# Kernel tuning notes

Hardware: AMD Instinct MI355X
Metric: run time of the kernel (lower is better)

## Reference

```python
import jax, jax.numpy as jnp
import numpy as np

N = 100000
E = 1600000

def _norms(src, dst):
    ones = jnp.ones(src.shape[0], dtype=jnp.float32)
    out_deg = jax.ops.segment_sum(ones, src, num_segments=N)
    in_deg = jax.ops.segment_sum(ones, dst, num_segments=N)
    # dgl clamps degree to >=1; with self-loops deg>=1 anyway
    out_norm = jax.lax.rsqrt(jnp.clip(out_deg, 1.0))
    in_norm = jax.lax.rsqrt(jnp.clip(in_deg, 1.0))
    return out_norm, in_norm

def _graph_conv(x, W, b, src, dst, out_norm, in_norm):
    h = (x * out_norm[:, None]) @ W          # [N, dout]
    msg = h[src]                              # gather  [E', dout]
    agg = jax.ops.segment_sum(msg, dst, num_segments=N)
    return agg * in_norm[:, None] + b

def setup_inputs() -> dict:
    key = jax.random.key(0)
    ks = jax.random.split(key, 8)
    feat = jax.random.normal(ks[0], (N, 128), dtype=jnp.float32)
    src = jax.random.randint(ks[1], (E,), 0, N, dtype=jnp.int32)
    dst = jax.random.randint(ks[2], (E,), 0, N, dtype=jnp.int32)
    s1 = 1.0 / np.sqrt(128.0)
    W1 = jax.random.uniform(ks[3], (128, 128), jnp.float32, -s1, s1)
    b1 = jnp.zeros((128,), jnp.float32)
    W2 = jax.random.uniform(ks[4], (128, 128), jnp.float32, -s1, s1)
    b2 = jnp.zeros((128,), jnp.float32)
    W3 = jax.random.uniform(ks[5], (128, 64), jnp.float32, -s1, s1)
    b3 = jnp.zeros((64,), jnp.float32)
    return {"feat": feat, "src": src, "dst": dst,
            "W1": W1, "b1": b1, "W2": W2, "b2": b2, "W3": W3, "b3": b3}

def reference(feat, src, dst, W1, b1, W2, b2, W3, b3):
    # dgl.add_self_loop
    loop = jnp.arange(N, dtype=src.dtype)
    s = jnp.concatenate([src, loop])
    d = jnp.concatenate([dst, loop])
    out_norm, in_norm = _norms(s, d)
    # dropout is identity in eval mode (deterministic reference)
    h = jax.nn.relu(_graph_conv(feat, W1, b1, s, d, out_norm, in_norm))
    h = jax.nn.relu(_graph_conv(h, W2, b2, s, d, out_norm, in_norm))
    h = _graph_conv(h, W3, b3, s, d, out_norm, in_norm)
    return h
```

## Files before the change

### kernel.cpp

```cpp
#include <hip/hip_runtime.h>
#include <hip/hip_fp16.h>


#define NFEAT 128
#define BBITS 8
#define BSZ 256
#define EPB 4096

union H8 { float4 f4; __half2 h2[4]; };

using half8v = __attribute__((ext_vector_type(8))) _Float16;
using f32x4  = __attribute__((ext_vector_type(4))) float;

__global__ __launch_bounds__(256) void hist_kernel(const int* __restrict__ src,
                                                   const int* __restrict__ dst,
                                                   int* __restrict__ hist2,
                                                   int NB, int nblk, int nh, int E) {
    __shared__ int hd[512], hs[512];
    const int t = threadIdx.x, b = blockIdx.x;
    for (int u = t; u < 512; u += 256) { hd[u] = 0; hs[u] = 0; }
    __syncthreads();
    const int base4 = b * (EPB / 4);
    #pragma unroll
    for (int j = 0; j < 4; ++j) {
        int i4 = base4 + j * 256 + t;
        int e0 = i4 * 4;
        if (e0 + 3 < E) {
            int4 s = ((const int4*)src)[i4];
            int4 d = ((const int4*)dst)[i4];
            atomicAdd(&hs[s.x >> BBITS], 1); atomicAdd(&hs[s.y >> BBITS], 1);
            atomicAdd(&hs[s.z >> BBITS], 1); atomicAdd(&hs[s.w >> BBITS], 1);
            atomicAdd(&hd[d.x >> BBITS], 1); atomicAdd(&hd[d.y >> BBITS], 1);
            atomicAdd(&hd[d.z >> BBITS], 1); atomicAdd(&hd[d.w >> BBITS], 1);
        } else {
            for (int e = e0; e < E && e < e0 + 4; ++e) {
                atomicAdd(&hs[src[e] >> BBITS], 1);
                atomicAdd(&hd[dst[e] >> BBITS], 1);
            }
        }
    }
    __syncthreads();
    for (int u = t; u < NB; u += 256) {
        hist2[u * nblk + b]      = hd[u];
        hist2[nh + u * nblk + b] = hs[u];
    }
}

__global__ __launch_bounds__(256) void scan1_kernel(int* __restrict__ data,
                                                    int* __restrict__ blk_sum, int n) {
    const int tid = threadIdx.x, lane = tid & 63, wid = tid >> 6;
    const int i2 = blockIdx.x * 256 + tid;
    int a = 0, b = 0;
    if (2 * i2 + 1 < n)      { int2 v = ((const int2*)data)[i2]; a = v.x; b = v.y; }
    else if (2 * i2 < n)     { a = data[2 * i2]; }
    int s = a + b;
    int incl = s;
    #pragma unroll
    for (int off = 1; off < 64; off <<= 1) {
        int t2 = __shfl_up(incl, off, 64);
        if (lane >= off) incl += t2;
    }
    __shared__ int ws[4];
    if (lane == 63) ws[wid] = incl;
    __syncthreads();
    int woff = 0;
    #pragma unroll
    for (int w = 0; w < 3; ++w) if (w < wid) woff += ws[w];
    int pref = woff + incl - s;
    if (2 * i2 < n)     data[2 * i2]     = pref;
    if (2 * i2 + 1 < n) data[2 * i2 + 1] = pref + a;
    if (tid == 0) blk_sum[blockIdx.x] = ws[0] + ws[1] + ws[2] + ws[3];
}

__global__ __launch_bounds__(1024) void scan2_kernel(int* __restrict__ blk, int nb) {
    const int tid = threadIdx.x, lane = tid & 63, wid = tid >> 6;
    int v = (tid < nb) ? blk[tid] : 0;
    int incl = v;
    #pragma unroll
    for (int off = 1; off < 64; off <<= 1) {
        int t = __shfl_up(incl, off, 64);
        if (lane >= off) incl += t;
    }
    __shared__ int ws[16];
    if (lane == 63) ws[wid] = incl;
    __syncthreads();
    int woff = 0;
    #pragma unroll
    for (int w = 0; w < 15; ++w) if (w < wid) woff += ws[w];
    if (tid < nb) blk[tid] = woff + incl - v;
}

__global__ __launch_bounds__(256) void scan3_kernel(int* __restrict__ data,
                                                    const int* __restrict__ blk, int n) {
    const int i2 = blockIdx.x * 256 + threadIdx.x;
    int add = blk[blockIdx.x];
    if (2 * i2 < n)     data[2 * i2]     += add;
    if (2 * i2 + 1 < n) data[2 * i2 + 1] += add;
}

__global__ __launch_bounds__(256) void scatter_kernel(const int* __restrict__ src,
                                                      const int* __restrict__ dst,
                                                      const int* __restrict__ hist2,
                                                      unsigned int* __restrict__ dstP,
                                                      unsigned char* __restrict__ srcB,
                                                      int NB, int nblk, int nh, int E) {
    __shared__ int hd[512], hs[512], baseD[512], baseS[512];
    const int t = threadIdx.x, b = blockIdx.x;
    for (int u = t; u < 512; u += 256) { hd[u] = 0; hs[u] = 0; }
    for (int u = t; u < NB; u += 256) {
        baseD[u] = hist2[u * nblk + b];
        baseS[u] = hist2[nh + u * nblk + b] - E;
    }
    __syncthreads();
    const int base4 = b * (EPB / 4);
    #pragma unroll
    for (int j = 0; j < 4; ++j) {
        int i4 = base4 + j * 256 + t;
        int e0 = i4 * 4;
        if (e0 + 3 < E) {
            int4 s = ((const int4*)src)[i4];
            int4 d = ((const int4*)dst)[i4];
            int se[4] = {s.x, s.y, s.z, s.w};
            int de[4] = {d.x, d.y, d.z, d.w};
            #pragma unroll
            for (int q = 0; q < 4; ++q) {
                int kd = de[q] >> BBITS;
                int pos = baseD[kd] + atomicAdd(&hd[kd], 1);
                dstP[pos] = ((unsigned int)(de[q] & (BSZ - 1)) << 24) | (unsigned int)se[q];
                int ks = se[q] >> BBITS;
                int posS = baseS[ks] + atomicAdd(&hs[ks], 1);
                srcB[posS] = (unsigned char)(se[q] & (BSZ - 1));
            }
        } else {
            for (int e = e0; e < E && e < e0 + 4; ++e) {
                int sv = src[e], dv = dst[e];
                int kd = dv >> BBITS;
                int pos = baseD[kd] + atomicAdd(&hd[kd], 1);
                dstP[pos] = ((unsigned int)(dv & (BSZ - 1)) << 24) | (unsigned int)sv;
                int ks = sv >> BBITS;
                int posS = baseS[ks] + atomicAdd(&hs[ks], 1);
                srcB[posS] = (unsigned char)(sv & (BSZ - 1));
            }
        }
    }
}

__global__ __launch_bounds__(256) void bucket_kernel(const unsigned int* __restrict__ dstP,
                                                     const unsigned char* __restrict__ srcB,
                                                     const int* __restrict__ hist2,
                                                     int* __restrict__ row_ptr,
                                                     int* __restrict__ col_idx,
                                                     float* __restrict__ in_norm,
                                                     float* __restrict__ out_norm,
                                                     int N, int NB, int nblk, int nh, int E) {
    __shared__ int cnt[BSZ], scnt[BSZ], start[BSZ], off[BSZ];
    __shared__ int ws[4];
    const int k = blockIdx.x, t = threadIdx.x;
    const int node0 = k << BBITS;
    cnt[t] = 0; scnt[t] = 0; off[t] = 0;
    __syncthreads();
    const int bB = hist2[k * nblk];
    const int bE = (k + 1 < NB) ? hist2[(k + 1) * nblk] : E;
    const int sB = hist2[nh + k * nblk] - E;
    const int sE = ((k + 1 < NB) ? hist2[nh + (k + 1) * nblk] : 2 * E) - E;
    for (int i = bB + t; i < bE; i += 256) atomicAdd(&cnt[dstP[i] >> 24], 1);
    for (int i = sB + t; i < sE; i += 256) atomicAdd(&scnt[srcB[i]], 1);
    __syncthreads();
    const int lane = t & 63, wid = t >> 6;
    int v = cnt[t];
    int incl = v;
    #pragma unroll
    for (int o = 1; o < 64; o <<= 1) {
        int x = __shfl_up(incl, o, 64);
        if (lane >= o) incl += x;
    }
    if (lane == 63) ws[wid] = incl;
    __syncthreads();
    int woff = 0;
    #pragma unroll
    for (int w = 0; w < 3; ++w) if (w < wid) woff += ws[w];
    start[t] = woff + incl - v;
    {
        int node = node0 + t;
        if (node < N) {
            row_ptr[node] = bB + start[t];
            in_norm[node]  = rsqrtf((float)(v + 1));
            out_norm[node] = rsqrtf((float)(scnt[t] + 1));
        }
    }
    if (k == 0 && t == 0) row_ptr[N] = E;
    __syncthreads();
    for (int i = bB + t; i < bE; i += 256) {
        unsigned int pv = dstP[i];
        int local = pv >> 24;
        int r = atomicAdd(&off[local], 1);
        col_idx[bB + start[local] + r] = (int)(pv & 0xFFFFFFu);
    }
}

__global__ void wt_all_kernel(const float* __restrict__ W1, const float* __restrict__ W2,
                              const float* __restrict__ W3, __half* __restrict__ Wt1,
                              __half* __restrict__ Wt2, __half* __restrict__ Wt3) {
    int b = blockIdx.x, k = threadIdx.x;
    if (b < 128)      Wt1[b * 128 + k] = __float2half(W1[k * 128 + b]);
    else if (b < 256) { int n = b - 128; Wt2[n * 128 + k] = __float2half(W2[k * 128 + n]); }
    else              { int n = b - 256; Wt3[n * 128 + k] = __float2half(W3[k * 64 + n]); }
}

template <int BN, typename XT>
__global__ __launch_bounds__(256) void mfma_gemm_kernel(const XT* __restrict__ x,
                                                        const __half* __restrict__ Wt,
                                                        const float* __restrict__ out_norm,
                                                        __half* __restrict__ h, int n_rows) {
    constexpr int BM = 64;
    constexpr int NT = BN / 16;
    __shared__ __half As[BM][136];
    __shared__ __half Bs[BN][136];
    const int tid  = threadIdx.x;
    const int row0 = blockIdx.x * BM;

    {
        int r  = tid >> 2;
        int c0 = (tid & 3) * 32;
        int grow = row0 + r;
        if (grow < n_rows) {
            float norm = out_norm[grow];
            if constexpr (sizeof(XT) == 4) {
                const float* xp = (const float*)x + (size_t)grow * NFEAT + c0;
                #pragma unroll
                for (int j = 0; j < 4; ++j) {
                    float4 p0 = *(const float4*)(xp + j * 8);
                    float4 p1 = *(const float4*)(xp + j * 8 + 4);
                    H8 u;
                    u.h2[0] = __floats2half2_rn(p0.x * norm, p0.y * norm);
                    u.h2[1] = __floats2half2_rn(p0.z * norm, p0.w * norm);
                    u.h2[2] = __floats2half2_rn(p1.x * norm, p1.y * norm);
                    u.h2[3] = __floats2half2_rn(p1.z * norm, p1.w * norm);
                    *(float4*)&As[r][c0 + j * 8] = u.f4;
                }
            } else {
                const __half* xp = (const __half*)x + (size_t)grow * NFEAT + c0;
                #pragma unroll
                for (int j = 0; j < 4; ++j) {
                    H8 u; u.f4 = *(const float4*)(xp + j * 8);
                    #pragma unroll
                    for (int q = 0; q < 4; ++q) {
                        float2 p = __half22float2(u.h2[q]);
                        u.h2[q] = __floats2half2_rn(p.x * norm, p.y * norm);
                    }
                    *(float4*)&As[r][c0 + j * 8] = u.f4;
                }
            }
        } else {
            H8 z; z.f4 = make_float4(0.f, 0.f, 0.f, 0.f);
            #pragma unroll
            for (int j = 0; j < 4; ++j) *(float4*)&As[r][c0 + j * 8] = z.f4;
        }
    }
    {
        constexpr int TPR = 256 / BN;
        constexpr int CH  = 128 / TPR;
        int wr = tid / TPR;
        int wc = (tid % TPR) * CH;
        const __half* wp = Wt + wr * 128 + wc;
        #pragma unroll
        for (int j = 0; j < CH / 8; ++j)
            *(float4*)&Bs[wr][wc + j * 8] = *(const float4*)(wp + j * 8);
    }
    __syncthreads();

    const int lane = tid & 63, wid = tid >> 6;
    const int lr = lane & 15, quad = lane >> 4;
    const int koff = quad * 8;
    f32x4 acc[NT];
    #pragma unroll
    for (int t = 0; t < NT; ++t) acc[t] = (f32x4){0.f, 0.f, 0.f, 0.f};

    #pragma unroll
    for (int ks = 0; ks < 4; ++ks) {
        half8v a = *(const half8v*)&As[wid * 16 + lr][ks * 32 + koff];
        #pragma unroll
        for (int nt = 0; nt < NT; ++nt) {
            half8v b = *(const half8v*)&Bs[nt * 16 + lr][ks * 32 + koff];
            acc[nt] = __builtin_amdgcn_mfma_f32_16x16x32_f16(a, b, acc[nt], 0, 0, 0);
        }
    }

    #pragma unroll
    for (int nt = 0; nt < NT; ++nt) {
        #pragma unroll
        for (int r = 0; r < 4; ++r) {
            int row = row0 + wid * 16 + quad * 4 + r;
            if (row < n_rows)
                h[(size_t)row * BN + nt * 16 + lr] = __float2half(acc[nt][r]);
        }
    }
}

template <int DOUT, bool RELU, typename OutT>
__global__ __launch_bounds__(256) void agg_kernel(const __half* __restrict__ h,
                                                  const int* __restrict__ row_ptr,
                                                  const int* __restrict__ col_idx,
                                                  const float* __restrict__ in_norm,
                                                  const float* __restrict__ bias,
                                                  OutT* __restrict__ out, int n) {
    constexpr int TPN = DOUT / 8;
    constexpr int NPB = 256 / TPN;
    const int tid  = threadIdx.x;
    const int sub  = tid / TPN;
    const int c    = (tid % TPN) * 8;
    const int node = blockIdx.x * NPB + sub;
    if (node >= n) return;

    float acc[8];
    {
        H8 u; u.f4 = *(const float4*)(h + (size_t)node * DOUT + c);
        #pragma unroll
        for (int q = 0; q < 4; ++q) {
            float2 p = __half22float2(u.h2[q]);
            acc[q * 2] = p.x; acc[q * 2 + 1] = p.y;
        }
    }
    int e  = row_ptr[node];
    int e1 = row_ptr[node + 1];
    for (; e + 3 < e1; e += 4) {
        int s0 = col_idx[e], s1 = col_idx[e + 1], s2 = col_idx[e + 2], s3 = col_idx[e + 3];
        H8 u0, u1, u2, u3;
        u0.f4 = *(const float4*)(h + (size_t)s0 * DOUT + c);
        u1.f4 = *(const float4*)(h + (size_t)s1 * DOUT + c);
        u2.f4 = *(const float4*)(h + (size_t)s2 * DOUT + c);
        u3.f4 = *(const float4*)(h + (size_t)s3 * DOUT + c);
        #pragma unroll
        for (int q = 0; q < 4; ++q) {
            float2 p0 = __half22float2(u0.h2[q]);
            float2 p1 = __half22float2(u1.h2[q]);
            float2 p2 = __half22float2(u2.h2[q]);
            float2 p3 = __half22float2(u3.h2[q]);
            acc[q * 2]     += (p0.x + p1.x) + (p2.x + p3.x);
            acc[q * 2 + 1] += (p0.y + p1.y) + (p2.y + p3.y);
        }
    }
    for (; e < e1; ++e) {
        int s0 = col_idx[e];
        H8 u0; u0.f4 = *(const float4*)(h + (size_t)s0 * DOUT + c);
        #pragma unroll
        for (int q = 0; q < 4; ++q) {
            float2 p0 = __half22float2(u0.h2[q]);
            acc[q * 2] += p0.x; acc[q * 2 + 1] += p0.y;
        }
    }
    float inn = in_norm[node];
    float r[8];
    #pragma unroll
    for (int q = 0; q < 8; ++q) {
        r[q] = acc[q] * inn + bias[c + q];
        if (RELU) r[q] = fmaxf(r[q], 0.0f);
    }
    if constexpr (sizeof(OutT) == 2) {
        H8 o;
        #pragma unroll
        for (int q = 0; q < 4; ++q) o.h2[q] = __floats2half2_rn(r[q * 2], r[q * 2 + 1]);
        *(float4*)((__half*)out + (size_t)node * DOUT + c) = o.f4;
    } else {
        float4 o0, o1;
        o0.x=r[0]; o0.y=r[1]; o0.z=r[2]; o0.w=r[3];
        o1.x=r[4]; o1.y=r[5]; o1.z=r[6]; o1.w=r[7];
        *(float4*)((float*)out + (size_t)node * DOUT + c)     = o0;
        *(float4*)((float*)out + (size_t)node * DOUT + c + 4) = o1;
    }
}

extern "C" void kernel_launch(void* const* d_in, const int* in_sizes, int n_in,
                              void* d_out, int out_size, void* d_ws, size_t ws_size,
                              hipStream_t stream) {
    const float* feat = (const float*)d_in[0];
    const int*   src  = (const int*)d_in[1];
    const int*   dst  = (const int*)d_in[2];
    const float* W1   = (const float*)d_in[3];
    const float* b1   = (const float*)d_in[4];
    const float* W2   = (const float*)d_in[5];
    const float* b2   = (const float*)d_in[6];
    const float* W3   = (const float*)d_in[7];
    const float* b3   = (const float*)d_in[8];

    const int N = in_sizes[0] / NFEAT;
    const int E = in_sizes[1];

    const int NB   = (N + BSZ - 1) / BSZ;
    const int nblk = (E + EPB - 1) / EPB;
    const int nh   = NB * nblk;
    const int n2   = 2 * nh;
    const int nsb  = (n2 + 511) / 512;

    char* ws = (char*)d_ws;
    auto alloc = [&](size_t bytes) {
        char* p = ws;
        ws += (bytes + 255) & ~(size_t)255;
        return p;
    };
    float* out_norm = (float*)alloc((size_t)N * 4);
    float* in_norm  = (float*)alloc((size_t)N * 4);
    int*   row_ptr  = (int*)alloc((size_t)(N + 1) * 4);
    int*   hist2    = (int*)alloc((size_t)n2 * 4);
    int*   blk_sum  = (int*)alloc((size_t)1024 * 4);
    __half* Wt1     = (__half*)alloc((size_t)128 * 128 * 2);
    __half* Wt2     = (__half*)alloc((size_t)128 * 128 * 2);
    __half* Wt3     = (__half*)alloc((size_t)64 * 128 * 2);
    int*   col_idx  = (int*)alloc((size_t)E * 4);
    __half* hA      = (__half*)alloc((size_t)N * NFEAT * 2);
    __half* hB      = (__half*)alloc((size_t)N * NFEAT * 2);
    unsigned int*  dstP = (unsigned int*)hA;
    unsigned char* srcB = (unsigned char*)(dstP + E);

    wt_all_kernel<<<320, 128, 0, stream>>>(W1, W2, W3, Wt1, Wt2, Wt3);

    hist_kernel<<<nblk, 256, 0, stream>>>(src, dst, hist2, NB, nblk, nh, E);
    scan1_kernel<<<nsb, 256, 0, stream>>>(hist2, blk_sum, n2);
    scan2_kernel<<<1, 1024, 0, stream>>>(blk_sum, nsb);
    scan3_kernel<<<nsb, 256, 0, stream>>>(hist2, blk_sum, n2);
    scatter_kernel<<<nblk, 256, 0, stream>>>(src, dst, hist2, dstP, srcB, NB, nblk, nh, E);
    bucket_kernel<<<NB, 256, 0, stream>>>(dstP, srcB, hist2, row_ptr, col_idx,
                                          in_norm, out_norm, N, NB, nblk, nh, E);

    const int gb = (N + 63) / 64;
    mfma_gemm_kernel<128, float><<<gb, 256, 0, stream>>>(feat, Wt1, out_norm, hA, N);
    agg_kernel<128, true, __half><<<(N + 15) / 16, 256, 0, stream>>>(hA, row_ptr, col_idx,
                                                                     in_norm, b1, hB, N);
    mfma_gemm_kernel<128, __half><<<gb, 256, 0, stream>>>(hB, Wt2, out_norm, hA, N);
    agg_kernel<128, true, __half><<<(N + 15) / 16, 256, 0, stream>>>(hA, row_ptr, col_idx,
                                                                     in_norm, b2, hB, N);
    mfma_gemm_kernel<64, __half><<<gb, 256, 0, stream>>>(hB, Wt3, out_norm, hA, N);
    agg_kernel<64, false, float><<<(N + 31) / 32, 256, 0, stream>>>(hA, row_ptr, col_idx,
                                                                    in_norm, b3, (float*)d_out, N);
}
```

Baseline: 357.2 us.

## Stage scatter through shared memory so global writes are bucket-contiguous

The radix scatter kernel now ranks each edge with local atomics, computes per-bucket local offsets with a block-wide scan, and reorders the edges in LDS before writing. The final global writes then go out in bucket-sorted order, so consecutive threads hit contiguous addresses instead of scattering randomly. The block size grows to 512 with about 36KB of LDS per block, which may reduce occupancy and adds extra syncs and scans. The kernel assumes NB is at most 512 buckets.

```diff
diff --git a/kernel.cpp b/kernel.cpp
--- a/kernel.cpp
+++ b/kernel.cpp
@@ -98,50 +98,104 @@
     if (2 * i2 + 1 < n) data[2 * i2 + 1] += add;
 }
 
-__global__ __launch_bounds__(256) void scatter_kernel(const int* __restrict__ src,
+__global__ __launch_bounds__(512) void scatter_kernel(const int* __restrict__ src,
                                                       const int* __restrict__ dst,
                                                       const int* __restrict__ hist2,
                                                       unsigned int* __restrict__ dstP,
                                                       unsigned char* __restrict__ srcB,
                                                       int NB, int nblk, int nh, int E) {
-    __shared__ int hd[512], hs[512], baseD[512], baseS[512];
+    __shared__ int hd[512], hs[512], startD[512], startS[512], baseD[512], baseS[512];
+    __shared__ int ws[8];
+    __shared__ unsigned int   payD[EPB];
+    __shared__ unsigned short kD[EPB];
+    __shared__ unsigned char  sV[EPB];
+    __shared__ unsigned short kS[EPB];
     const int t = threadIdx.x, b = blockIdx.x;
-    for (int u = t; u < 512; u += 256) { hd[u] = 0; hs[u] = 0; }
-    for (int u = t; u < NB; u += 256) {
+    const int lane = t & 63, wid = t >> 6;
+    hd[t] = 0; hs[t] = 0;
+    for (int u = t; u < NB; u += 512) {
         baseD[u] = hist2[u * nblk + b];
         baseS[u] = hist2[nh + u * nblk + b] - E;
     }
     __syncthreads();
-    const int base4 = b * (EPB / 4);
-    #pragma unroll
-    for (int j = 0; j < 4; ++j) {
-        int i4 = base4 + j * 256 + t;
-        int e0 = i4 * 4;
-        if (e0 + 3 < E) {
-            int4 s = ((const int4*)src)[i4];
-            int4 d = ((const int4*)dst)[i4];
-            int se[4] = {s.x, s.y, s.z, s.w};
-            int de[4] = {d.x, d.y, d.z, d.w};
-            #pragma unroll
-            for (int q = 0; q < 4; ++q) {
-                int kd = de[q] >> BBITS;
-                int pos = baseD[kd] + atomicAdd(&hd[kd], 1);
-                dstP[pos] = ((unsigned int)(de[q] & (BSZ - 1)) << 24) | (unsigned int)se[q];
-                int ks = se[q] >> BBITS;
-                int posS = baseS[ks] + atomicAdd(&hs[ks], 1);
-                srcB[posS] = (unsigned char)(se[q] & (BSZ - 1));
-            }
-        } else {
-            for (int e = e0; e < E && e < e0 + 4; ++e) {
-                int sv = src[e], dv = dst[e];
-                int kd = dv >> BBITS;
-                int pos = baseD[kd] + atomicAdd(&hd[kd], 1);
-                dstP[pos] = ((unsigned int)(dv & (BSZ - 1)) << 24) | (unsigned int)sv;
-                int ks = sv >> BBITS;
-                int posS = baseS[ks] + atomicAdd(&hs[ks], 1);
-                srcB[posS] = (unsigned char)(sv & (BSZ - 1));
-            }
-        }
+
+    const int e0 = b * EPB;
+    const int nE = min(EPB, E - e0);
+    int se[8], de[8], rD[8], rS[8];
+    const int be = e0 + t * 8;
+    if (be + 7 < E) {
+        int4 s0 = ((const int4*)src)[(be >> 2)];
+        int4 s1 = ((const int4*)src)[(be >> 2) + 1];
+        int4 d0 = ((const int4*)dst)[(be >> 2)];
+        int4 d1 = ((const int4*)dst)[(be >> 2) + 1];
+        se[0]=s0.x; se[1]=s0.y; se[2]=s0.z; se[3]=s0.w;
+        se[4]=s1.x; se[5]=s1.y; se[6]=s1.z; se[7]=s1.w;
+        de[0]=d0.x; de[1]=d0.y; de[2]=d0.z; de[3]=d0.w;
+        de[4]=d1.x; de[5]=d1.y; de[6]=d1.z; de[7]=d1.w;
+    } else {
+        #pragma unroll
+        for (int j = 0; j < 8; ++j) {
+            se[j] = (be + j < E) ? src[be + j] : 0;
+            de[j] = (be + j < E) ? dst[be + j] : 0;
+        }
+    }
+    #pragma unroll
+    for (int j = 0; j < 8; ++j) {
+        if (be + j < E) {
+            rD[j] = atomicAdd(&hd[de[j] >> BBITS], 1);
+            rS[j] = atomicAdd(&hs[se[j] >> BBITS], 1);
+        }
+    }
+    __syncthreads();
+    {
+        int v = hd[t], incl = v;
+        #pragma unroll
+        for (int o = 1; o < 64; o <<= 1) {
+            int x = __shfl_up(incl, o, 64);
+            if (lane >= o) incl += x;
+        }
+        if (lane == 63) ws[wid] = incl;
+        __syncthreads();
+        int woff = 0;
+        #pragma unroll
+        for (int w = 0; w < 7; ++w) if (w < wid) woff += ws[w];
+        startD[t] = woff + incl - v;
+    }
+    __syncthreads();
+    {
+        int v = hs[t], incl = v;
+        #pragma unroll
+        for (int o = 1; o < 64; o <<= 1) {
+            int x = __shfl_up(incl, o, 64);
+            if (lane >= o) incl += x;
+        }
+        if (lane == 63) ws[wid] = incl;
+        __syncthreads();
+        int woff = 0;
+        #pragma unroll
+        for (int w = 0; w < 7; ++w) if (w < wid) woff += ws[w];
+        startS[t] = woff + incl - v;
+    }
+    __syncthreads();
+    #pragma unroll
+    for (int j = 0; j < 8; ++j) {
+        if (be + j < E) {
+            int kd = de[j] >> BBITS;
+            int p  = startD[kd] + rD[j];
+            payD[p] = ((unsigned int)(de[j] & (BSZ - 1)) << 24) | (unsigned int)se[j];
+            kD[p]   = (unsigned short)kd;
+            int ks = se[j] >> BBITS;
+            int q  = startS[ks] + rS[j];
+            sV[q] = (unsigned char)(se[j] & (BSZ - 1));
+            kS[q] = (unsigned short)ks;
+        }
+    }
+    __syncthreads();
+    for (int p = t; p < nE; p += 512) {
+        int k = kD[p];
+        dstP[baseD[k] + (p - startD[k])] = payD[p];
+        int k2 = kS[p];
+        srcB[baseS[k2] + (p - startS[k2])] = sV[p];
     }
 }
 
@@ -418,7 +472,7 @@
     scan1_kernel<<<nsb, 256, 0, stream>>>(hist2, blk_sum, n2);
     scan2_kernel<<<1, 1024, 0, stream>>>(blk_sum, nsb);
     scan3_kernel<<<nsb, 256, 0, stream>>>(hist2, blk_sum, n2);
-    scatter_kernel<<<nblk, 256, 0, stream>>>(src, dst, hist2, dstP, srcB, NB, nblk, nh, E);
+    scatter_kernel<<<nblk, 512, 0, stream>>>(src, dst, hist2, dstP, srcB, NB, nblk, nh, E);
     bucket_kernel<<<NB, 256, 0, stream>>>(dstP, srcB, hist2, row_ptr, col_idx,
                                           in_norm, out_norm, N, NB, nblk, nh, E);
 
```

Measured after the change: 345.9 us. 1.03x faster.
